# Performance work log

Hardware: AMD Instinct MI355X
Metric: run time of the kernel (lower is better)

The kernel has to match this reference:

```python
import jax, jax.numpy as jnp
import numpy as np

QUERY_DIM = 512
KEY_DIM = 512
NUM_HEADS = 16
HEAD_DIM = QUERY_DIM // NUM_HEADS


def setup_inputs() -> dict:
    key = jax.random.key(0)
    ks = jax.random.split(key, 10)
    B, T, S = 4, 2048, 2048
    s_q = 1.0 / np.sqrt(QUERY_DIM)
    s_k = 1.0 / np.sqrt(KEY_DIM)
    return {
        "x": jax.random.normal(ks[0], (B, T, QUERY_DIM), dtype=jnp.float32),
        "context": jax.random.normal(ks[1], (B, S, KEY_DIM), dtype=jnp.float32),
        "Wq": jax.random.normal(ks[2], (QUERY_DIM, QUERY_DIM), dtype=jnp.float32) * s_q,
        "bq": jnp.zeros((QUERY_DIM,), dtype=jnp.float32),
        "Wk": jax.random.normal(ks[3], (KEY_DIM, QUERY_DIM), dtype=jnp.float32) * s_k,
        "bk": jnp.zeros((QUERY_DIM,), dtype=jnp.float32),
        "Wv": jax.random.normal(ks[4], (KEY_DIM, QUERY_DIM), dtype=jnp.float32) * s_k,
        "bv": jnp.zeros((QUERY_DIM,), dtype=jnp.float32),
        "Wo": jax.random.normal(ks[5], (QUERY_DIM, QUERY_DIM), dtype=jnp.float32) * s_q,
        "bo": jnp.zeros((QUERY_DIM,), dtype=jnp.float32),
    }


def reference(x, context, Wq, bq, Wk, bk, Wv, bv, Wo, bo):
    B, T, C = x.shape
    S = context.shape[1]
    H, D = NUM_HEADS, HEAD_DIM
    scale = D ** -0.5
    # projections -> [B, H, T/S, D]
    q = (x @ Wq + bq).reshape(B, T, H, D).transpose(0, 2, 1, 3)
    k = (context @ Wk + bk).reshape(B, S, H, D).transpose(0, 2, 1, 3)
    v = (context @ Wv + bv).reshape(B, S, H, D).transpose(0, 2, 1, 3)
    # explicit attention matrix [B, H, T, S] (faithful to the unfused original)
    attn = jnp.einsum("bhtd,bhsd->bhts", q, k) * scale
    attn = jax.nn.softmax(attn, axis=-1)  # dropout is identity in eval mode
    out = jnp.einsum("bhts,bhsd->bhtd", attn, v)
    out = out.transpose(0, 2, 1, 3).reshape(B, T, C)
    return out @ Wo + bo
```

## Files before the change

kernel.cpp:

```cpp
#include <hip/hip_runtime.h>
#include <hip/hip_bf16.h>
#include <cmath>

typedef __bf16 bf16;
typedef __bf16 bf16x2 __attribute__((ext_vector_type(2)));
typedef __bf16 bf16x4 __attribute__((ext_vector_type(4)));
typedef __bf16 bf16x8 __attribute__((ext_vector_type(8)));
typedef float floatx4 __attribute__((ext_vector_type(4)));
typedef unsigned int uintx2 __attribute__((ext_vector_type(2)));
typedef unsigned int uintx4 __attribute__((ext_vector_type(4)));

#define MFMA_BF16(a, b, c) __builtin_amdgcn_mfma_f32_16x16x32_bf16((a), (b), (c), 0, 0, 0)

#if defined(__has_builtin)
#if __has_builtin(__builtin_amdgcn_global_load_lds)
#define HAVE_GLL 1
#endif
#if __has_builtin(__builtin_amdgcn_cvt_pk_bf16_f32)
#define HAVE_PKCVT 1
#endif
#if __has_builtin(__builtin_amdgcn_permlane32_swap) && __has_builtin(__builtin_amdgcn_permlane16_swap)
#define HAVE_PLSWAP 1
#endif
#endif

__device__ __forceinline__ void stage16(const bf16* g, bf16* ldsbase, int lane) {
#ifdef HAVE_GLL
    __builtin_amdgcn_global_load_lds((const __attribute__((address_space(1))) unsigned int*)g,
                                     (__attribute__((address_space(3))) unsigned int*)ldsbase,
                                     16, 0, 0);
#else
    *(int4*)(ldsbase + lane * 8) = *(const int4*)g;
#endif
}

__device__ __forceinline__ unsigned pk2(float a, float b) {
    bf16x2 t;
#ifdef HAVE_PKCVT
    t = __builtin_amdgcn_cvt_pk_bf16_f32(a, b);
#else
    t[0] = (bf16)a;
    t[1] = (bf16)b;
#endif
    return __builtin_bit_cast(unsigned, t);
}

__device__ __forceinline__ uintx2 p32swap(unsigned x, unsigned y) {
#ifdef HAVE_PLSWAP
    auto r = __builtin_amdgcn_permlane32_swap(x, y, false, false);
    uintx2 o;
    o[0] = r[0];
    o[1] = r[1];
    return o;
#else
    const int lane = threadIdx.x & 63;
    const unsigned px = __shfl(x, lane ^ 32);
    const unsigned py = __shfl(y, lane ^ 32);
    uintx2 o;
    o[0] = (lane & 32) ? py : x;
    o[1] = (lane & 32) ? y : px;
    return o;
#endif
}

__device__ __forceinline__ uintx2 p16swap(unsigned x, unsigned y) {
#ifdef HAVE_PLSWAP
    auto r = __builtin_amdgcn_permlane16_swap(x, y, false, false);
    uintx2 o;
    o[0] = r[0];
    o[1] = r[1];
    return o;
#else
    const int lane = threadIdx.x & 63;
    const unsigned px = __shfl(x, lane ^ 16);
    const unsigned py = __shfl(y, lane ^ 16);
    uintx2 o;
    o[0] = (lane & 16) ? py : x;
    o[1] = (lane & 16) ? y : px;
    return o;
#endif
}

__device__ __forceinline__ int detect_bf16(const void* x) {
    const unsigned short* u = (const unsigned short*)x;
    const int lane = threadIdx.x & 63;
    const unsigned short w0 = u[4 * lane], w1 = u[4 * lane + 2];
    const int e0 = (w0 >> 7) & 0xFF, e1 = (w1 >> 7) & 0xFF;
    const unsigned long long b0 = __ballot(e0 >= 96 && e0 <= 158);
    const unsigned long long b1 = __ballot(e1 >= 96 && e1 <= 158);
    return (__popcll(b0) + __popcll(b1)) >= 90;
}

struct PrepArgs {
    const void* x;
    const void* ctx;
    const void* W[4];
    const void* bias[4];
    bf16* xc;
    bf16* ctxc;
    bf16* WT[4];
    bf16* biasc;
};

__global__ __launch_bounds__(256) void prep(PrepArgs a) {
    const int tid = threadIdx.x;
    const int f = detect_bf16(a.x);
    const int bid = blockIdx.x;
    if (bid < 1024) {
        const int w = bid >> 8, tileid = bid & 255;
        const int bx = tileid & 15, by = tileid >> 4;
        const void* __restrict__ in = a.W[w];
        bf16* __restrict__ out = a.WT[w];
        __shared__ bf16 tile[32][33];
        const int tx = tid & 31, ty = tid >> 5;
        const int x = bx * 32 + tx;
        const int y0 = by * 32;
#pragma unroll
        for (int yy = ty; yy < 32; yy += 8) {
            const size_t idx = (size_t)(y0 + yy) * 512 + x;
            const float v = f ? (float)((const bf16*)in)[idx] : ((const float*)in)[idx];
            tile[yy][tx] = (bf16)v;
        }
        __syncthreads();
        const int xo = by * 32 + tx;
        const int y1 = bx * 32;
#pragma unroll
        for (int yy = ty; yy < 32; yy += 8)
            out[(size_t)(y1 + yy) * 512 + xo] = tile[tx][yy];
    } else if (bid < 5120) {
        if (f) return;
        const int seg = (bid >= 3072);
        const void* src = seg ? a.ctx : a.x;
        bf16* dst = seg ? a.ctxc : a.xc;
        const int off = (bid - (seg ? 3072 : 1024)) * 256 + tid;
        const float4 p = ((const float4*)src)[2 * off];
        const float4 q = ((const float4*)src)[2 * off + 1];
        bf16x8 o;
        o[0] = (bf16)p.x; o[1] = (bf16)p.y; o[2] = (bf16)p.z; o[3] = (bf16)p.w;
        o[4] = (bf16)q.x; o[5] = (bf16)q.y; o[6] = (bf16)q.z; o[7] = (bf16)q.w;
        *(bf16x8*)(dst + (size_t)off * 8) = o;
    } else {
        for (int e = tid; e < 2048; e += 256) {
            const int seg = e >> 9, off = e & 511;
            const float v =
                f ? (float)((const bf16*)a.bias[seg])[off] : ((const float*)a.bias[seg])[off];
            a.biasc[seg * 512 + off] = (bf16)v;
        }
    }
}

struct QkvArgs {
    const void* xraw;
    const void* ctxraw;
    const bf16* Aconv[3];
    const bf16* Wt[3];
    const bf16* bias;
    bf16* out[3];
    float scale[3];
};

__global__ __launch_bounds__(256) void gemm_qkv(QkvArgs a) {
    __shared__ __align__(16) bf16 lA[128 * 32];
    __shared__ __align__(16) bf16 lB[128 * 32];
    const int z = blockIdx.z;
    const int f = detect_bf16(a.xraw);
    const bf16* __restrict__ A =
        f ? (const bf16*)(z == 0 ? a.xraw : a.ctxraw) : a.Aconv[z];
    const bf16* __restrict__ Wt = a.Wt[z];
    const int tid = threadIdx.x, wave = tid >> 6, lane = tid & 63;
    const int qd = lane >> 4, j = lane & 15;
    const int m0 = blockIdx.x * 128, n0 = blockIdx.y * 128;
    const int wrow = (wave & 1) * 64, wcol = (wave >> 1) * 64;
    const int srow = wave * 16 + (lane >> 2);
    const int scol = (lane & 3) * 8;
    const bf16* agp = A + (size_t)(m0 + srow) * 512 + scol;
    const bf16* bgp = Wt + (size_t)(n0 + srow) * 512 + scol;
    bf16* lA0 = lA + wave * 512;
    bf16* lB0 = lB + wave * 512;

    floatx4 acc[4][4] = {};

    for (int k0 = 0; k0 < 512; k0 += 32) {
        stage16(agp + k0, lA0, lane);
        stage16(agp + k0 + (size_t)64 * 512, lA0 + 64 * 32, lane);
        stage16(bgp + k0, lB0, lane);
        stage16(bgp + k0 + (size_t)64 * 512, lB0 + 64 * 32, lane);
        __syncthreads();
        bf16x8 af[4], bfr[4];
#pragma unroll
        for (int i = 0; i < 4; ++i) {
            af[i] = *(const bf16x8*)(lA + (wrow + i * 16 + j) * 32 + qd * 8);
            bfr[i] = *(const bf16x8*)(lB + (wcol + i * 16 + j) * 32 + qd * 8);
        }
        if (z < 2) {
#pragma unroll
            for (int nt = 0; nt < 4; ++nt)
#pragma unroll
                for (int rf = 0; rf < 4; ++rf)
                    acc[nt][rf] = MFMA_BF16(bfr[nt], af[rf], acc[nt][rf]);
        } else {
#pragma unroll
            for (int rf = 0; rf < 4; ++rf)
#pragma unroll
                for (int nt = 0; nt < 4; ++nt)
                    acc[rf][nt] = MFMA_BF16(af[rf], bfr[nt], acc[rf][nt]);
        }
        __syncthreads();
    }

    const float scale = a.scale[z];
    const bf16* bias = a.bias + z * 512;
    bf16* __restrict__ C = a.out[z];
    if (z < 2) {
#pragma unroll
        for (int nt = 0; nt < 4; ++nt) {
            const int nb = n0 + wcol + nt * 16 + qd * 4;
            const bf16x4 bv4 = *(const bf16x4*)(bias + nb);
            const int h = nb >> 5, d0 = nb & 31;
#pragma unroll
            for (int rf = 0; rf < 4; ++rf) {
                const int m = m0 + wrow + rf * 16 + j;
                const int bb = m >> 11, t = m & 2047;
                bf16x4 pk;
#pragma unroll
                for (int r = 0; r < 4; ++r)
                    pk[r] = (bf16)((acc[nt][rf][r] + (float)bv4[r]) * scale);
                *(bf16x4*)(&C[(((size_t)bb * 16 + h) * 2048 + t) * 32 + d0]) = pk;
            }
        }
    } else {
#pragma unroll
        for (int nt = 0; nt < 4; ++nt) {
            const int n = n0 + wcol + nt * 16 + j;
            const float bv = (float)bias[n];
            const int h = n >> 5, d = n & 31;
#pragma unroll
            for (int rf = 0; rf < 4; ++rf) {
                const int t0 = m0 + wrow + rf * 16 + qd * 4;
                const int bb = t0 >> 11, s = t0 & 2047;
                bf16x4 pk;
#pragma unroll
                for (int r = 0; r < 4; ++r) pk[r] = (bf16)(acc[rf][nt][r] + bv);
                *(bf16x4*)(&C[(((size_t)bb * 16 + h) * 32 + d) * 2048 + s]) = pk;
            }
        }
    }
}

__device__ __forceinline__ void gll16kv(const bf16* g, bf16* lds) {
#ifdef HAVE_GLL
    __builtin_amdgcn_global_load_lds((const __attribute__((address_space(1))) unsigned int*)g,
                                     (__attribute__((address_space(3))) unsigned int*)lds,
                                     16, 0, 0);
#else
    *(int4*)(lds + (threadIdx.x & 63) * 8) = *(const int4*)g;
#endif
}

__global__ __launch_bounds__(256, 4) void attn_kernel(const bf16* __restrict__ Q,
                                                      const bf16* __restrict__ Kh,
                                                      const bf16* __restrict__ Vt,
                                                      bf16* __restrict__ O) {
    const int tid = threadIdx.x;
    const int wave = tid >> 6, lane = tid & 63;
    const int qd = lane >> 4, j = lane & 15;
    const int bh = blockIdx.x;
    const int b = bh >> 4, h = bh & 15;
    const int tw = blockIdx.y * 128 + wave * 32;

    __shared__ __align__(16) bf16 lsK[2][2][2048];
    __shared__ __align__(16) bf16 lsV[2][2][2048];

    const bf16* qbase = Q + ((size_t)bh * 2048 + tw) * 32;
    const bf16* kbase = Kh + (size_t)bh * 2048 * 32;
    const bf16* vbase = Vt + (size_t)bh * 32 * 2048;

    bf16x8 qf[2];
#pragma unroll
    for (int tf = 0; tf < 2; ++tf)
        qf[tf] = *(const bf16x8*)(qbase + (size_t)(tf * 16 + j) * 32 + qd * 8);

    const bf16* ksrc = kbase + (size_t)(wave * 16 + j) * 32 + qd * 8;
    const bf16* vsrc =
        vbase + (size_t)((wave >> 1) * 16 + j) * 2048 + (wave & 1) * 32 + qd * 8;
    bf16* kdst = &lsK[0][0][wave * 512];
    bf16* vdst = &lsV[0][0][wave * 512];

    auto stage = [&](int buf, int s0) {
        gll16kv(ksrc + (size_t)s0 * 32, kdst + buf * 4096);
        gll16kv(ksrc + (size_t)(s0 + 64) * 32, kdst + buf * 4096 + 2048);
        gll16kv(vsrc + s0, vdst + buf * 4096);
        gll16kv(vsrc + s0 + 64, vdst + buf * 4096 + 2048);
    };

    bf16x8 ones;
#pragma unroll
    for (int e = 0; e < 8; ++e) ones[e] = (bf16)1.0f;

    const floatx4 zero = {0.f, 0.f, 0.f, 0.f};
    floatx4 oacc[2][2] = {};
    floatx4 dacc[2] = {};

    auto qk = [&](const bf16* lk, bf16x8* pf) {
        bf16x8 kf[4];
#pragma unroll
        for (int sf = 0; sf < 4; ++sf)
            kf[sf] = *(const bf16x8*)(lk + sf * 512 + lane * 8);
#pragma unroll
        for (int tf = 0; tf < 2; ++tf) {
            floatx4 sc[4];
#pragma unroll
            for (int sf = 0; sf < 4; ++sf) sc[sf] = MFMA_BF16(kf[sf], qf[tf], zero);
            unsigned SW[4][2];
#pragma unroll
            for (int sf = 0; sf < 4; ++sf) {
                const float e0 = __builtin_amdgcn_exp2f(sc[sf][0]);
                const float e1 = __builtin_amdgcn_exp2f(sc[sf][1]);
                const float e2 = __builtin_amdgcn_exp2f(sc[sf][2]);
                const float e3 = __builtin_amdgcn_exp2f(sc[sf][3]);
                SW[sf][0] = pk2(e0, e1);
                SW[sf][1] = pk2(e2, e3);
            }
            const uintx2 a0 = p32swap(SW[0][0], SW[1][0]);
            const uintx2 a1 = p32swap(SW[0][1], SW[1][1]);
            const uintx2 c0 = p32swap(SW[2][0], SW[3][0]);
            const uintx2 c1 = p32swap(SW[2][1], SW[3][1]);
            const uintx2 t0 = p16swap(a0[0], a0[1]);
            const uintx2 t1 = p16swap(a1[0], a1[1]);
            const uintx2 t2 = p16swap(c0[0], c0[1]);
            const uintx2 t3 = p16swap(c1[0], c1[1]);
            uintx4 w0, w1;
            w0[0] = t0[0]; w0[1] = t1[0]; w0[2] = t0[1]; w0[3] = t1[1];
            w1[0] = t2[0]; w1[1] = t3[0]; w1[2] = t2[1]; w1[3] = t3[1];
            pf[tf * 2 + 0] = __builtin_bit_cast(bf16x8, w0);
            pf[tf * 2 + 1] = __builtin_bit_cast(bf16x8, w1);
        }
    };
    auto pv = [&](const bf16* lv, const bf16x8* pf) {
        bf16x8 vf[4];
#pragma unroll
        for (int i = 0; i < 4; ++i)
            vf[i] = *(const bf16x8*)(lv + i * 512 + lane * 8);
#pragma unroll
        for (int tf = 0; tf < 2; ++tf) {
            oacc[tf][0] = MFMA_BF16(pf[tf * 2 + 0], vf[0], oacc[tf][0]);
            oacc[tf][1] = MFMA_BF16(pf[tf * 2 + 0], vf[2], oacc[tf][1]);
            dacc[tf] = MFMA_BF16(pf[tf * 2 + 0], ones, dacc[tf]);
            oacc[tf][0] = MFMA_BF16(pf[tf * 2 + 1], vf[1], oacc[tf][0]);
            oacc[tf][1] = MFMA_BF16(pf[tf * 2 + 1], vf[3], oacc[tf][1]);
            dacc[tf] = MFMA_BF16(pf[tf * 2 + 1], ones, dacc[tf]);
        }
    };

    stage(0, 0);

    int cur = 0;
#pragma unroll 1
    for (int ph = 0; ph < 16; ++ph) {
        if (ph < 15) {
            stage(cur ^ 1, (ph + 1) * 128);
            asm volatile("s_waitcnt vmcnt(4)" ::: "memory");
        } else {
            asm volatile("s_waitcnt vmcnt(0)" ::: "memory");
        }
        __builtin_amdgcn_sched_barrier(0);
        __builtin_amdgcn_s_barrier();
        __builtin_amdgcn_sched_barrier(0);

        bf16x8 pfA[4], pfB[4];
        qk(&lsK[cur][0][0], pfA);
        qk(&lsK[cur][1][0], pfB);
        pv(&lsV[cur][0][0], pfA);
        pv(&lsV[cur][1][0], pfB);

        __builtin_amdgcn_sched_barrier(0);
        __builtin_amdgcn_s_barrier();
        __builtin_amdgcn_sched_barrier(0);
        cur ^= 1;
    }

#pragma unroll
    for (int tf = 0; tf < 2; ++tf)
#pragma unroll
        for (int r = 0; r < 4; ++r) {
            const float inv = 1.0f / dacc[tf][r];
            const int t = tw + tf * 16 + qd * 4 + r;
#pragma unroll
            for (int dt = 0; dt < 2; ++dt)
                O[((size_t)b * 2048 + t) * 512 + h * 32 + dt * 16 + j] =
                    (bf16)(oacc[tf][dt][r] * inv);
        }
}

__global__ __launch_bounds__(256) void gemm_out(const bf16* __restrict__ A,
                                                const bf16* __restrict__ Wt,
                                                const bf16* __restrict__ bias,
                                                void* __restrict__ C,
                                                const void* __restrict__ xraw) {
    __shared__ __align__(16) bf16 lA[128 * 32];
    __shared__ __align__(16) bf16 lB[128 * 32];
    const int oflag = detect_bf16(xraw);
    const int tid = threadIdx.x, wave = tid >> 6, lane = tid & 63;
    const int qd = lane >> 4, j = lane & 15;
    const int m0 = blockIdx.x * 128, n0 = blockIdx.y * 128;
    const int wrow = (wave & 1) * 64, wcol = (wave >> 1) * 64;
    const int srow = wave * 16 + (lane >> 2);
    const int scol = (lane & 3) * 8;
    const bf16* agp = A + (size_t)(m0 + srow) * 512 + scol;
    const bf16* bgp = Wt + (size_t)(n0 + srow) * 512 + scol;
    bf16* lA0 = lA + wave * 512;
    bf16* lB0 = lB + wave * 512;

    floatx4 acc[4][4] = {};

    for (int k0 = 0; k0 < 512; k0 += 32) {
        stage16(agp + k0, lA0, lane);
        stage16(agp + k0 + (size_t)64 * 512, lA0 + 64 * 32, lane);
        stage16(bgp + k0, lB0, lane);
        stage16(bgp + k0 + (size_t)64 * 512, lB0 + 64 * 32, lane);
        __syncthreads();
        bf16x8 af[4], bfr[4];
#pragma unroll
        for (int i = 0; i < 4; ++i) {
            af[i] = *(const bf16x8*)(lA + (wrow + i * 16 + j) * 32 + qd * 8);
            bfr[i] = *(const bf16x8*)(lB + (wcol + i * 16 + j) * 32 + qd * 8);
        }
#pragma unroll
        for (int nt = 0; nt < 4; ++nt)
#pragma unroll
            for (int rf = 0; rf < 4; ++rf)
                acc[nt][rf] = MFMA_BF16(bfr[nt], af[rf], acc[nt][rf]);
        __syncthreads();
    }

#pragma unroll
    for (int nt = 0; nt < 4; ++nt) {
        const int nb = n0 + wcol + nt * 16 + qd * 4;
        const bf16x4 bv4 = *(const bf16x4*)(bias + nb);
#pragma unroll
        for (int rf = 0; rf < 4; ++rf) {
            const int m = m0 + wrow + rf * 16 + j;
            if (oflag) {
                bf16x4 pk;
#pragma unroll
                for (int r = 0; r < 4; ++r) pk[r] = (bf16)(acc[nt][rf][r] + (float)bv4[r]);
                *(bf16x4*)((bf16*)C + (size_t)m * 512 + nb) = pk;
            } else {
                float4 v;
                v.x = acc[nt][rf][0] + (float)bv4[0];
                v.y = acc[nt][rf][1] + (float)bv4[1];
                v.z = acc[nt][rf][2] + (float)bv4[2];
                v.w = acc[nt][rf][3] + (float)bv4[3];
                *(float4*)((float*)C + (size_t)m * 512 + nb) = v;
            }
        }
    }
}

extern "C" void kernel_launch(void* const* d_in, const int* in_sizes, int n_in, void* d_out,
                              int out_size, void* d_ws, size_t ws_size, hipStream_t stream) {
    char* ws = (char*)d_ws;
    bf16* wqT = (bf16*)(ws + 1048576);
    bf16* wkT = (bf16*)(ws + 1572864);
    bf16* wvT = (bf16*)(ws + 2097152);
    bf16* woT = (bf16*)(ws + 2621440);
    bf16* biasc = (bf16*)(ws + 3145728);
    bf16* xc = (bf16*)(ws + 4194304);
    bf16* ctxc = (bf16*)(ws + 12582912);
    bf16* qws = (bf16*)(ws + 20971520);
    bf16* kws = (bf16*)(ws + 29360128);
    bf16* vtws = (bf16*)(ws + 37748736);
    bf16* aws = xc;

    PrepArgs pa;
    pa.x = d_in[0]; pa.ctx = d_in[1];
    pa.W[0] = d_in[2]; pa.W[1] = d_in[4]; pa.W[2] = d_in[6]; pa.W[3] = d_in[8];
    pa.bias[0] = d_in[3]; pa.bias[1] = d_in[5]; pa.bias[2] = d_in[7]; pa.bias[3] = d_in[9];
    pa.xc = xc; pa.ctxc = ctxc;
    pa.WT[0] = wqT; pa.WT[1] = wkT; pa.WT[2] = wvT; pa.WT[3] = woT;
    pa.biasc = biasc;
    prep<<<5121, 256, 0, stream>>>(pa);

    QkvArgs qa;
    qa.xraw = d_in[0]; qa.ctxraw = d_in[1];
    qa.Aconv[0] = xc; qa.Aconv[1] = ctxc; qa.Aconv[2] = ctxc;
    qa.Wt[0] = wqT; qa.Wt[1] = wkT; qa.Wt[2] = wvT;
    qa.bias = biasc;
    qa.out[0] = qws; qa.out[1] = kws; qa.out[2] = vtws;
    qa.scale[0] = 0.2550348593f; qa.scale[1] = 1.0f; qa.scale[2] = 1.0f;
    gemm_qkv<<<dim3(64, 4, 3), 256, 0, stream>>>(qa);

    attn_kernel<<<dim3(64, 16), 256, 0, stream>>>(qws, kws, vtws, aws);

    gemm_out<<<dim3(64, 4), 256, 0, stream>>>(aws, woT, biasc + 3 * 512, d_out, d_in[0]);
}
```

Before: 194.1 us.

## Double-buffer LDS staging in QKV and output projection GEMMs

Both projection GEMM kernels now keep two LDS buffers and issue the global-to-LDS loads for the next K tile before computing on the current one. Explicit vmcnt waits and s_barrier calls wrapped in sched_barrier replace the two __syncthreads, so load latency can overlap the MFMA work. This doubles LDS use per block, which may lower occupancy. It also relies on stage16 issuing exactly four outstanding vector memory ops per stage for the vmcnt(4) wait to be correct.

```diff
diff --git a/kernel.cpp b/kernel.cpp
--- a/kernel.cpp
+++ b/kernel.cpp
@@ -160,8 +160,8 @@
 };
 
 __global__ __launch_bounds__(256) void gemm_qkv(QkvArgs a) {
-    __shared__ __align__(16) bf16 lA[128 * 32];
-    __shared__ __align__(16) bf16 lB[128 * 32];
+    __shared__ __align__(16) bf16 lA[2][128 * 32];
+    __shared__ __align__(16) bf16 lB[2][128 * 32];
     const int z = blockIdx.z;
     const int f = detect_bf16(a.xraw);
     const bf16* __restrict__ A =
@@ -175,22 +175,35 @@
     const int scol = (lane & 3) * 8;
     const bf16* agp = A + (size_t)(m0 + srow) * 512 + scol;
     const bf16* bgp = Wt + (size_t)(n0 + srow) * 512 + scol;
-    bf16* lA0 = lA + wave * 512;
-    bf16* lB0 = lB + wave * 512;
+
+    auto stage = [&](int buf, int k0) {
+        stage16(agp + k0, &lA[buf][wave * 512], lane);
+        stage16(agp + k0 + (size_t)64 * 512, &lA[buf][wave * 512 + 2048], lane);
+        stage16(bgp + k0, &lB[buf][wave * 512], lane);
+        stage16(bgp + k0 + (size_t)64 * 512, &lB[buf][wave * 512 + 2048], lane);
+    };
 
     floatx4 acc[4][4] = {};
 
-    for (int k0 = 0; k0 < 512; k0 += 32) {
-        stage16(agp + k0, lA0, lane);
-        stage16(agp + k0 + (size_t)64 * 512, lA0 + 64 * 32, lane);
-        stage16(bgp + k0, lB0, lane);
-        stage16(bgp + k0 + (size_t)64 * 512, lB0 + 64 * 32, lane);
-        __syncthreads();
+    stage(0, 0);
+    int cur = 0;
+#pragma unroll 1
+    for (int it = 0; it < 16; ++it) {
+        if (it < 15) {
+            stage(cur ^ 1, (it + 1) * 32);
+            asm volatile("s_waitcnt vmcnt(4)" ::: "memory");
+        } else {
+            asm volatile("s_waitcnt vmcnt(0)" ::: "memory");
+        }
+        __builtin_amdgcn_sched_barrier(0);
+        __builtin_amdgcn_s_barrier();
+        __builtin_amdgcn_sched_barrier(0);
+
         bf16x8 af[4], bfr[4];
 #pragma unroll
         for (int i = 0; i < 4; ++i) {
-            af[i] = *(const bf16x8*)(lA + (wrow + i * 16 + j) * 32 + qd * 8);
-            bfr[i] = *(const bf16x8*)(lB + (wcol + i * 16 + j) * 32 + qd * 8);
+            af[i] = *(const bf16x8*)(&lA[cur][(wrow + i * 16 + j) * 32 + qd * 8]);
+            bfr[i] = *(const bf16x8*)(&lB[cur][(wcol + i * 16 + j) * 32 + qd * 8]);
         }
         if (z < 2) {
 #pragma unroll
@@ -205,7 +218,11 @@
                 for (int nt = 0; nt < 4; ++nt)
                     acc[rf][nt] = MFMA_BF16(af[rf], bfr[nt], acc[rf][nt]);
         }
-        __syncthreads();
+
+        __builtin_amdgcn_sched_barrier(0);
+        __builtin_amdgcn_s_barrier();
+        __builtin_amdgcn_sched_barrier(0);
+        cur ^= 1;
     }
 
     const float scale = a.scale[z];
@@ -397,8 +414,8 @@
                                                 const bf16* __restrict__ bias,
                                                 void* __restrict__ C,
                                                 const void* __restrict__ xraw) {
-    __shared__ __align__(16) bf16 lA[128 * 32];
-    __shared__ __align__(16) bf16 lB[128 * 32];
+    __shared__ __align__(16) bf16 lA[2][128 * 32];
+    __shared__ __align__(16) bf16 lB[2][128 * 32];
     const int oflag = detect_bf16(xraw);
     const int tid = threadIdx.x, wave = tid >> 6, lane = tid & 63;
     const int qd = lane >> 4, j = lane & 15;
@@ -408,29 +425,46 @@
     const int scol = (lane & 3) * 8;
     const bf16* agp = A + (size_t)(m0 + srow) * 512 + scol;
     const bf16* bgp = Wt + (size_t)(n0 + srow) * 512 + scol;
-    bf16* lA0 = lA + wave * 512;
-    bf16* lB0 = lB + wave * 512;
+
+    auto stage = [&](int buf, int k0) {
+        stage16(agp + k0, &lA[buf][wave * 512], lane);
+        stage16(agp + k0 + (size_t)64 * 512, &lA[buf][wave * 512 + 2048], lane);
+        stage16(bgp + k0, &lB[buf][wave * 512], lane);
+        stage16(bgp + k0 + (size_t)64 * 512, &lB[buf][wave * 512 + 2048], lane);
+    };
 
     floatx4 acc[4][4] = {};
 
-    for (int k0 = 0; k0 < 512; k0 += 32) {
-        stage16(agp + k0, lA0, lane);
-        stage16(agp + k0 + (size_t)64 * 512, lA0 + 64 * 32, lane);
-        stage16(bgp + k0, lB0, lane);
-        stage16(bgp + k0 + (size_t)64 * 512, lB0 + 64 * 32, lane);
-        __syncthreads();
+    stage(0, 0);
+    int cur = 0;
+#pragma unroll 1
+    for (int it = 0; it < 16; ++it) {
+        if (it < 15) {
+            stage(cur ^ 1, (it + 1) * 32);
+            asm volatile("s_waitcnt vmcnt(4)" ::: "memory");
+        } else {
+            asm volatile("s_waitcnt vmcnt(0)" ::: "memory");
+        }
+        __builtin_amdgcn_sched_barrier(0);
+        __builtin_amdgcn_s_barrier();
+        __builtin_amdgcn_sched_barrier(0);
+
         bf16x8 af[4], bfr[4];
 #pragma unroll
         for (int i = 0; i < 4; ++i) {
-            af[i] = *(const bf16x8*)(lA + (wrow + i * 16 + j) * 32 + qd * 8);
-            bfr[i] = *(const bf16x8*)(lB + (wcol + i * 16 + j) * 32 + qd * 8);
+            af[i] = *(const bf16x8*)(&lA[cur][(wrow + i * 16 + j) * 32 + qd * 8]);
+            bfr[i] = *(const bf16x8*)(&lB[cur][(wcol + i * 16 + j) * 32 + qd * 8]);
         }
 #pragma unroll
         for (int nt = 0; nt < 4; ++nt)
 #pragma unroll
             for (int rf = 0; rf < 4; ++rf)
                 acc[nt][rf] = MFMA_BF16(bfr[nt], af[rf], acc[nt][rf]);
-        __syncthreads();
+
+        __builtin_amdgcn_sched_barrier(0);
+        __builtin_amdgcn_s_barrier();
+        __builtin_amdgcn_sched_barrier(0);
+        cur ^= 1;
     }
 
 #pragma unroll
```

Result: no change. 197.6 us (+1.8%).
